# Optimization experiments

Hardware: AMD Instinct MI355X
Metric: run time of the kernel (lower is better)

## Reference

```python
import jax, jax.numpy as jnp
import numpy as np

CH, G, K, STRIDE, RR = 256, 16, 7, 1, 4
GROUP = CH // G            # channels per group
PAD = (K - 1) // 2
BN_EPS = 1e-5


def setup_inputs() -> dict:
    key = jax.random.key(0)
    ks = jax.random.split(key, 9)
    b, dim = 16, 4096
    hid = CH // RR  # 64
    return {
        "x": jax.random.normal(ks[0], (b, CH, dim), jnp.float32),
        "w1": jax.random.normal(ks[1], (hid, CH), jnp.float32) * (1.0 / np.sqrt(CH)),
        "b1": jax.random.normal(ks[2], (hid,), jnp.float32) * 0.02,
        "bn_gamma": 1.0 + 0.1 * jax.random.normal(ks[3], (hid,), jnp.float32),
        "bn_beta": 0.1 * jax.random.normal(ks[4], (hid,), jnp.float32),
        "bn_mean": 0.1 * jax.random.normal(ks[5], (hid,), jnp.float32),
        "bn_var": jax.random.uniform(ks[6], (hid,), jnp.float32) + 0.5,
        "w2": jax.random.normal(ks[7], (K * G, hid), jnp.float32) * (1.0 / np.sqrt(hid)),
        "b2": jax.random.normal(ks[8], (K * G,), jnp.float32) * 0.02,
    }


def _involution(x, w1, b1, bn_gamma, bn_beta, bn_mean, bn_var, w2, b2):
    b, ch, dim = x.shape
    L = dim // STRIDE  # out_dim
    # unfold: pad then gather K shifted strided views -> [b, ch, K, L]
    xp = jnp.pad(x, ((0, 0), (0, 0), (PAD, PAD)))
    unfolded = jnp.stack(
        [xp[:, :, k : k + STRIDE * (L - 1) + 1 : STRIDE] for k in range(K)], axis=2
    )
    unfolded = unfolded.reshape(b, G, GROUP, K, L)
    # adaptive max pool to L (windows of size STRIDE); identity when STRIDE == 1
    pooled = x.reshape(b, ch, L, STRIDE).max(axis=-1)
    # kernel generator: 1x1 conv -> relu -> batchnorm (inference) -> 1x1 conv
    h = jnp.einsum("oc,bcl->bol", w1, pooled) + b1[:, None]
    h = jax.nn.relu(h)
    h = (h - bn_mean[:, None]) * jax.lax.rsqrt(bn_var[:, None] + BN_EPS)
    h = h * bn_gamma[:, None] + bn_beta[:, None]
    kern = jnp.einsum("oc,bcl->bol", w2, h) + b2[:, None]  # [b, K*G, L]
    kern = kern.reshape(b, G, K, L)
    # per-location dynamic kernel multiply + reduce over K
    out = jnp.einsum("bgkl,bgckl->bgcl", kern, unfolded)
    return out.reshape(b, ch, L)


def reference(x, w1, b1, bn_gamma, bn_beta, bn_mean, bn_var, w2, b2):
    return _involution(x, w1, b1, bn_gamma, bn_beta, bn_mean, bn_var, w2, b2)
```

## Files before the change

### kernel.cpp

```cpp
#include <hip/hip_runtime.h>

#define BB   16
#define CHN  256
#define DIMN 4096
#define KK   7
#define PADK 3
#define HID  64
#define KGN  112
#define TLC  128
#define XSTD 69
#define HSTH 138
#define KSTD 132
#define BN_EPS 1e-5f

typedef __fp16 half2_t __attribute__((ext_vector_type(2)));
typedef __fp16 half8   __attribute__((ext_vector_type(8)));
typedef float  f32x4   __attribute__((ext_vector_type(4)));

union U32H2 { unsigned int u; half2_t h; };

static __device__ __forceinline__ unsigned int packf(float a, float b) {
    U32H2 t; t.h = __builtin_amdgcn_cvt_pkrtz(a, b); return t.u;
}
static __device__ __forceinline__ half2_t ash2(unsigned int u) { U32H2 t; t.u = u; return t.h; }
static __device__ __forceinline__ __fp16 u16h(unsigned short u) {
    return __builtin_bit_cast(__fp16, u);
}
static __device__ __forceinline__ unsigned short hu16(__fp16 h) {
    return __builtin_bit_cast(unsigned short, h);
}

__global__ __launch_bounds__(256) void setup_k(
    const float* __restrict__ w1, const float* __restrict__ w2,
    const float* __restrict__ bn_gamma, const float* __restrict__ bn_beta,
    const float* __restrict__ bn_mean,  const float* __restrict__ bn_var,
    __fp16* __restrict__ w1f, __fp16* __restrict__ w2f,
    float* __restrict__ scb, float* __restrict__ shb) {
    int t = blockIdx.x * 256 + threadIdx.x;
    if (t < HID * CHN) w1f[t] = (__fp16)w1[t];
    if (t < KGN * HID) w2f[t] = (__fp16)w2[t];
    if (t < HID) {
        float s = bn_gamma[t] * rsqrtf(bn_var[t] + BN_EPS);
        scb[t] = s;
        shb[t] = bn_beta[t] - bn_mean[t] * s;
    }
}

template <int OFF>
static __device__ __forceinline__ void extract2(const uint2 q[4],
                                                float kva[KK], float kvb[KK]) {
#pragma unroll
    for (int k = 0; k < KK; ++k) {
        const int kk = k + OFF;
        const int i  = kk >> 1;
        const int h  = kk & 1;
        half2_t a = ash2(q[i].x);
        half2_t c = ash2(q[i].y);
        kva[k] = h ? (float)a[1] : (float)a[0];
        kvb[k] = h ? (float)c[1] : (float)c[0];
    }
}

__global__ __launch_bounds__(512, 2) void fused_k(
    const float* __restrict__ x,
    const __fp16* __restrict__ w1f,
    const float* __restrict__ b1,
    const float* __restrict__ scb, const float* __restrict__ shb,
    const __fp16* __restrict__ w2f,
    const float* __restrict__ b2,
    float* __restrict__ out) {
    __shared__ unsigned int   xs[CHN * XSTD];
    __shared__ unsigned short hs[HID * HSTH];
    __shared__ unsigned int   ks[56 * KSTD];

    const int t    = threadIdx.x;
    const int lane = t & 63;
    const int w    = t >> 6;
    const int lr   = t & 15;
    const int lg   = (t >> 4) & 3;
    const int b    = blockIdx.x >> 5;
    const int l0   = (blockIdx.x & 31) * TLC;

    unsigned short* xs16 = (unsigned short*)xs;

    {
        const int c  = t & 31;
        const int rr = t >> 5;
        const float* xg = x + ((size_t)b * CHN + rr) * DIMN + l0 + 4 * c;
#pragma unroll 4
        for (int rd = 0; rd < 16; ++rd) {
            const int row = 16 * rd + rr;
            float4 v = *(const float4*)(xg + (size_t)(16 * rd) * DIMN);
            unsigned int* dst = xs + row * XSTD + 2 * c + 2;
            dst[0] = packf(v.x, v.y);
            dst[1] = packf(v.z, v.w);
        }
        const int row  = t >> 1;
        const int side = t & 1;
        const float* xrow = x + ((size_t)b * CHN + row) * DIMN;
        if (side == 0) {
#pragma unroll
            for (int j = 0; j < 3; ++j) {
                int dc = l0 - 3 + j;
                float v = (dc >= 0) ? xrow[dc] : 0.0f;
                xs16[row * (2 * XSTD) + 1 + j] = hu16((__fp16)v);
            }
        } else {
#pragma unroll
            for (int j = 0; j < 3; ++j) {
                int dc = l0 + TLC + j;
                float v = (dc < DIMN) ? xrow[dc] : 0.0f;
                xs16[row * (2 * XSTD) + 132 + j] = hu16((__fp16)v);
            }
        }
    }
    __syncthreads();

    const int colL = 16 * w + lr;

    f32x4 acc[4];
#pragma unroll
    for (int of = 0; of < 4; ++of) acc[of] = (f32x4){0.f, 0.f, 0.f, 0.f};

#pragma unroll
    for (int p = 0; p < 8; ++p) {
        half8 bf;
#pragma unroll
        for (int j = 0; j < 8; ++j)
            bf[j] = u16h(xs16[(32 * p + 8 * lg + j) * (2 * XSTD) + colL + 4]);
#pragma unroll
        for (int of = 0; of < 4; ++of) {
            half8 af = *(const half8*)(w1f + (16 * of + lr) * CHN + 32 * p + 8 * lg);
            acc[of] = __builtin_amdgcn_mfma_f32_16x16x32_f16(af, bf, acc[of], 0, 0, 0);
        }
    }

#pragma unroll
    for (int of = 0; of < 4; ++of) {
#pragma unroll
        for (int r = 0; r < 4; ++r) {
            const int o = 16 * of + 4 * lg + r;
            float hv = fmaxf(acc[of][r] + b1[o], 0.f) * scb[o] + shb[o];
            hs[o * HSTH + colL] = hu16((__fp16)hv);
        }
    }

    f32x4 acc2[7];
#pragma unroll
    for (int rf = 0; rf < 7; ++rf) acc2[rf] = (f32x4){0.f, 0.f, 0.f, 0.f};

#pragma unroll
    for (int kx = 0; kx < 2; ++kx) {
        half8 bf;
#pragma unroll
        for (int j = 0; j < 8; ++j)
            bf[j] = u16h(hs[(32 * kx + 8 * lg + j) * HSTH + colL]);
#pragma unroll
        for (int rf = 0; rf < 7; ++rf) {
            half8 af = *(const half8*)(w2f + (16 * rf + lr) * HID + 32 * kx + 8 * lg);
            acc2[rf] = __builtin_amdgcn_mfma_f32_16x16x32_f16(af, bf, acc2[rf], 0, 0, 0);
        }
    }

#pragma unroll
    for (int rf = 0; rf < 7; ++rf) {
#pragma unroll
        for (int p = 0; p < 2; ++p) {
            const int r0 = 16 * rf + 4 * lg + 2 * p;
            float k0 = acc2[rf][2 * p + 0] + b2[r0 + 0];
            float k1 = acc2[rf][2 * p + 1] + b2[r0 + 1];
            ks[(r0 >> 1) * KSTD + colL] = packf(k0, k1);
        }
    }
    __syncthreads();

    const int l  = lane;
    const int c0 = 2 * l;
    float* outp = out + ((size_t)b * CHN + 32 * w) * DIMN + l0 + c0;

#pragma unroll
    for (int gi = 0; gi < 2; ++gi) {
        const int g   = 2 * w + gi;
        const int rpb = (7 * g) >> 1;
        uint2 q[4];
#pragma unroll
        for (int ii = 0; ii < 4; ++ii)
            q[ii] = *(const uint2*)(ks + (rpb + ii) * KSTD + c0);
        float kva[KK], kvb[KK];
        if (gi == 0) extract2<0>(q, kva, kvb);
        else         extract2<1>(q, kva, kvb);

#pragma unroll 8
        for (int i2 = 0; i2 < 16; ++i2) {
            const int ch = 32 * w + 16 * gi + i2;
            const unsigned int* xr = xs + ch * XSTD + l;
            unsigned int uu[5];
#pragma unroll
            for (int j = 0; j < 5; ++j) uu[j] = xr[j];
            float xv[8];
#pragma unroll
            for (int r = 1; r <= 8; ++r) {
                unsigned int u = uu[r >> 1];
                unsigned short us = (r & 1) ? (unsigned short)(u >> 16)
                                            : (unsigned short)(u & 0xffff);
                xv[r - 1] = (float)u16h(us);
            }
            float o0 = 0.f, o1 = 0.f;
#pragma unroll
            for (int k = 0; k < KK; ++k) {
                o0 = fmaf(kva[k], xv[k],     o0);
                o1 = fmaf(kvb[k], xv[k + 1], o1);
            }
            *(float2*)(outp + (size_t)(16 * gi + i2) * DIMN) = make_float2(o0, o1);
        }
    }
}

extern "C" void kernel_launch(void* const* d_in, const int* in_sizes, int n_in,
                              void* d_out, int out_size, void* d_ws, size_t ws_size,
                              hipStream_t stream) {
    (void)in_sizes; (void)n_in; (void)out_size; (void)ws_size;

    const float* x        = (const float*)d_in[0];
    const float* w1       = (const float*)d_in[1];
    const float* b1       = (const float*)d_in[2];
    const float* bn_gamma = (const float*)d_in[3];
    const float* bn_beta  = (const float*)d_in[4];
    const float* bn_mean  = (const float*)d_in[5];
    const float* bn_var   = (const float*)d_in[6];
    const float* w2       = (const float*)d_in[7];
    const float* b2       = (const float*)d_in[8];
    float*       out      = (float*)d_out;

    __fp16* w1f = (__fp16*)d_ws;
    __fp16* w2f = w1f + HID * CHN;
    float*  scb = (float*)(w2f + KGN * HID);
    float*  shb = scb + HID;

    setup_k<<<(HID * CHN + 255) / 256, 256, 0, stream>>>(
        w1, w2, bn_gamma, bn_beta, bn_mean, bn_var, w1f, w2f, scb, shb);
    fused_k<<<BB * (DIMN / TLC), 512, 0, stream>>>(
        x, w1f, b1, scb, shb, w2f, b2, out);
}
```

Measured before the change: 61.85 us.

## Stream x through double-buffered LDS panels and reread x from global in involution

Shrinks the LDS staging of x from the full 256-channel tile to two 32-channel panels, double-buffered and prefetched from global memory while the first-layer MFMA runs. This cuts shared memory per block so the launch bound can rise to 4 blocks per SM for more occupancy. The involution stage now reads x again from global (float4 with halo, relying on L2 hits) and computes 4 outputs per lane with float4 stores, in fp32 instead of fp16-rounded x. The cost is more global traffic and extra barriers in the panel loop.

```diff
diff --git a/kernel.cpp b/kernel.cpp
--- a/kernel.cpp
+++ b/kernel.cpp
@@ -8,7 +8,9 @@
 #define HID  64
 #define KGN  112
 #define TLC  128
-#define XSTD 69
+#define NPAN 8
+#define PCH  32
+#define XSTD 66
 #define HSTH 138
 #define KSTD 132
 #define BN_EPS 1e-5f
@@ -47,21 +49,22 @@
 }
 
 template <int OFF>
-static __device__ __forceinline__ void extract2(const uint2 q[4],
-                                                float kva[KK], float kvb[KK]) {
+static __device__ __forceinline__ void extract_kv(const uint4 q[4], float kv[KK][4]) {
 #pragma unroll
     for (int k = 0; k < KK; ++k) {
         const int kk = k + OFF;
         const int i  = kk >> 1;
         const int h  = kk & 1;
-        half2_t a = ash2(q[i].x);
-        half2_t c = ash2(q[i].y);
-        kva[k] = h ? (float)a[1] : (float)a[0];
-        kvb[k] = h ? (float)c[1] : (float)c[0];
-    }
-}
-
-__global__ __launch_bounds__(512, 2) void fused_k(
+#pragma unroll
+        for (int j = 0; j < 4; ++j) {
+            unsigned int u = (&q[i].x)[j];
+            half2_t hh = ash2(u);
+            kv[k][j] = h ? (float)hh[1] : (float)hh[0];
+        }
+    }
+}
+
+__global__ __launch_bounds__(512, 4) void fused_k(
     const float* __restrict__ x,
     const __fp16* __restrict__ w1f,
     const float* __restrict__ b1,
@@ -69,7 +72,7 @@
     const __fp16* __restrict__ w2f,
     const float* __restrict__ b2,
     float* __restrict__ out) {
-    __shared__ unsigned int   xs[CHN * XSTD];
+    __shared__ unsigned int   xs[2][PCH * XSTD];
     __shared__ unsigned short hs[HID * HSTH];
     __shared__ unsigned int   ks[56 * KSTD];
 
@@ -80,58 +83,58 @@
     const int lg   = (t >> 4) & 3;
     const int b    = blockIdx.x >> 5;
     const int l0   = (blockIdx.x & 31) * TLC;
-
-    unsigned short* xs16 = (unsigned short*)xs;
-
-    {
-        const int c  = t & 31;
-        const int rr = t >> 5;
-        const float* xg = x + ((size_t)b * CHN + rr) * DIMN + l0 + 4 * c;
-#pragma unroll 4
-        for (int rd = 0; rd < 16; ++rd) {
-            const int row = 16 * rd + rr;
-            float4 v = *(const float4*)(xg + (size_t)(16 * rd) * DIMN);
-            unsigned int* dst = xs + row * XSTD + 2 * c + 2;
-            dst[0] = packf(v.x, v.y);
-            dst[1] = packf(v.z, v.w);
-        }
-        const int row  = t >> 1;
-        const int side = t & 1;
-        const float* xrow = x + ((size_t)b * CHN + row) * DIMN;
-        if (side == 0) {
-#pragma unroll
-            for (int j = 0; j < 3; ++j) {
-                int dc = l0 - 3 + j;
-                float v = (dc >= 0) ? xrow[dc] : 0.0f;
-                xs16[row * (2 * XSTD) + 1 + j] = hu16((__fp16)v);
+    const int colL = 16 * w + lr;
+
+    const unsigned short* xs16[2] = {
+        (const unsigned short*)xs[0], (const unsigned short*)xs[1] };
+
+    const int colq = t & 31;
+    const int chl  = t >> 5;
+    const float* xg = x + ((size_t)b * CHN + chl) * DIMN + l0 + 4 * colq;
+
+    float4 pre[2];
+#pragma unroll
+    for (int i = 0; i < 2; ++i)
+        pre[i] = *(const float4*)(xg + (size_t)(16 * i) * DIMN);
+#pragma unroll
+    for (int i = 0; i < 2; ++i) {
+        uint2 v;
+        v.x = packf(pre[i].x, pre[i].y);
+        v.y = packf(pre[i].z, pre[i].w);
+        *(uint2*)&xs[0][(chl + 16 * i) * XSTD + 2 * colq] = v;
+    }
+    __syncthreads();
+
+    f32x4 acc[4];
+#pragma unroll
+    for (int of = 0; of < 4; ++of) acc[of] = (f32x4){0.f, 0.f, 0.f, 0.f};
+
+    for (int p = 0; p < NPAN; ++p) {
+        if (p + 1 < NPAN) {
+#pragma unroll
+            for (int i = 0; i < 2; ++i)
+                pre[i] = *(const float4*)(xg + (size_t)(32 * (p + 1) + 16 * i) * DIMN);
+        }
+        const unsigned short* xb = xs16[p & 1];
+        half8 bf;
+#pragma unroll
+        for (int j = 0; j < 8; ++j)
+            bf[j] = u16h(xb[(8 * lg + j) * (2 * XSTD) + colL]);
+#pragma unroll
+        for (int of = 0; of < 4; ++of) {
+            half8 af = *(const half8*)(w1f + (16 * of + lr) * CHN + PCH * p + 8 * lg);
+            acc[of] = __builtin_amdgcn_mfma_f32_16x16x32_f16(af, bf, acc[of], 0, 0, 0);
+        }
+        if (p + 1 < NPAN) {
+            __syncthreads();
+#pragma unroll
+            for (int i = 0; i < 2; ++i) {
+                uint2 v;
+                v.x = packf(pre[i].x, pre[i].y);
+                v.y = packf(pre[i].z, pre[i].w);
+                *(uint2*)&xs[(p + 1) & 1][(chl + 16 * i) * XSTD + 2 * colq] = v;
             }
-        } else {
-#pragma unroll
-            for (int j = 0; j < 3; ++j) {
-                int dc = l0 + TLC + j;
-                float v = (dc < DIMN) ? xrow[dc] : 0.0f;
-                xs16[row * (2 * XSTD) + 132 + j] = hu16((__fp16)v);
-            }
-        }
-    }
-    __syncthreads();
-
-    const int colL = 16 * w + lr;
-
-    f32x4 acc[4];
-#pragma unroll
-    for (int of = 0; of < 4; ++of) acc[of] = (f32x4){0.f, 0.f, 0.f, 0.f};
-
-#pragma unroll
-    for (int p = 0; p < 8; ++p) {
-        half8 bf;
-#pragma unroll
-        for (int j = 0; j < 8; ++j)
-            bf[j] = u16h(xs16[(32 * p + 8 * lg + j) * (2 * XSTD) + colL + 4]);
-#pragma unroll
-        for (int of = 0; of < 4; ++of) {
-            half8 af = *(const half8*)(w1f + (16 * of + lr) * CHN + 32 * p + 8 * lg);
-            acc[of] = __builtin_amdgcn_mfma_f32_16x16x32_f16(af, bf, acc[of], 0, 0, 0);
+            __syncthreads();
         }
     }
 
@@ -174,44 +177,44 @@
     }
     __syncthreads();
 
-    const int l  = lane;
-    const int c0 = 2 * l;
-    float* outp = out + ((size_t)b * CHN + 32 * w) * DIMN + l0 + c0;
+    const int q4   = lane & 31;
+    const int hi   = lane >> 5;
+    const int col0 = l0 + 4 * q4;
 
 #pragma unroll
     for (int gi = 0; gi < 2; ++gi) {
         const int g   = 2 * w + gi;
         const int rpb = (7 * g) >> 1;
-        uint2 q[4];
+        uint4 qq[4];
 #pragma unroll
         for (int ii = 0; ii < 4; ++ii)
-            q[ii] = *(const uint2*)(ks + (rpb + ii) * KSTD + c0);
-        float kva[KK], kvb[KK];
-        if (gi == 0) extract2<0>(q, kva, kvb);
-        else         extract2<1>(q, kva, kvb);
-
-#pragma unroll 8
-        for (int i2 = 0; i2 < 16; ++i2) {
-            const int ch = 32 * w + 16 * gi + i2;
-            const unsigned int* xr = xs + ch * XSTD + l;
-            unsigned int uu[5];
-#pragma unroll
-            for (int j = 0; j < 5; ++j) uu[j] = xr[j];
-            float xv[8];
-#pragma unroll
-            for (int r = 1; r <= 8; ++r) {
-                unsigned int u = uu[r >> 1];
-                unsigned short us = (r & 1) ? (unsigned short)(u >> 16)
-                                            : (unsigned short)(u & 0xffff);
-                xv[r - 1] = (float)u16h(us);
+            qq[ii] = *(const uint4*)(ks + (rpb + ii) * KSTD + 4 * q4);
+        float kv[KK][4];
+        if (gi == 0) extract_kv<0>(qq, kv);
+        else         extract_kv<1>(qq, kv);
+
+#pragma unroll 4
+        for (int i2 = 0; i2 < 8; ++i2) {
+            const int ch = 32 * w + 16 * gi + 2 * i2 + hi;
+            const float* xrow = x + ((size_t)b * CHN + ch) * DIMN;
+            float4 fa = *(const float4*)(xrow + (col0 > 0 ? col0 - 4 : 0));
+            float4 fb = *(const float4*)(xrow + col0);
+            float4 fc = *(const float4*)(xrow + (col0 + 4 < DIMN ? col0 + 4 : DIMN - 4));
+
+            float xr[10] = { fa.y, fa.z, fa.w, fb.x, fb.y, fb.z, fb.w, fc.x, fc.y, fc.z };
+            if (col0 == 0)        { xr[0] = 0.f; xr[1] = 0.f; xr[2] = 0.f; }
+            if (col0 == DIMN - 4) { xr[7] = 0.f; xr[8] = 0.f; xr[9] = 0.f; }
+
+            float o0 = 0.f, o1 = 0.f, o2 = 0.f, o3 = 0.f;
+#pragma unroll
+            for (int k = 0; k < KK; ++k) {
+                o0 = fmaf(kv[k][0], xr[k + 0], o0);
+                o1 = fmaf(kv[k][1], xr[k + 1], o1);
+                o2 = fmaf(kv[k][2], xr[k + 2], o2);
+                o3 = fmaf(kv[k][3], xr[k + 3], o3);
             }
-            float o0 = 0.f, o1 = 0.f;
-#pragma unroll
-            for (int k = 0; k < KK; ++k) {
-                o0 = fmaf(kva[k], xv[k],     o0);
-                o1 = fmaf(kvb[k], xv[k + 1], o1);
-            }
-            *(float2*)(outp + (size_t)(16 * gi + i2) * DIMN) = make_float2(o0, o1);
+            *(float4*)(out + ((size_t)b * CHN + ch) * DIMN + col0) =
+                make_float4(o0, o1, o2, o3);
         }
     }
 }
```

Measured after the change: 76.30 us. 23.4% more time.
